# Optimization experiments

Measured on AMD Instinct MI355X. Metric: run time of the kernel, lower is better.

## Reference

```python
import jax, jax.numpy as jnp
import numpy as np

N = 65536      # points
NS = 16        # nsample
CIN = 128
CMID = 128
COUT = 128
S = 8          # share_planes
EPS = 1e-5


def setup_inputs() -> dict:
    key = jax.random.key(0)
    ks = jax.random.split(key, 12)
    f = lambda k, shape, s=0.05: (jax.random.normal(k, shape, jnp.float32) * s)
    inp = {
        'p': jax.random.normal(ks[0], (N, 3), jnp.float32),
        'x': jax.random.normal(ks[1], (N, CIN), jnp.float32),
        'idx': jax.random.randint(ks[2], (N, NS), 0, N, jnp.int32),
        'wq': f(ks[3], (CMID, CIN)), 'bq': jnp.zeros((CMID,), jnp.float32),
        'wk': f(ks[4], (CMID, CIN)), 'bk': jnp.zeros((CMID,), jnp.float32),
        'wv': f(ks[5], (COUT, CIN)), 'bv': jnp.zeros((COUT,), jnp.float32),
        'p_w1': f(ks[6], (3, 3), 0.3), 'p_b1': jnp.zeros((3,), jnp.float32),
        'p_bng': jnp.ones((3,), jnp.float32), 'p_bnb': jnp.zeros((3,), jnp.float32),
        'p_bnm': jnp.zeros((3,), jnp.float32), 'p_bnv': jnp.ones((3,), jnp.float32),
        'p_w2': f(ks[7], (COUT, 3), 0.3), 'p_b2': jnp.zeros((COUT,), jnp.float32),
        'w_bn1g': jnp.ones((CMID,), jnp.float32), 'w_bn1b': jnp.zeros((CMID,), jnp.float32),
        'w_bn1m': jnp.zeros((CMID,), jnp.float32), 'w_bn1v': jnp.ones((CMID,), jnp.float32),
        'w_w1': f(ks[8], (CMID // S, CMID)), 'w_b1': jnp.zeros((CMID // S,), jnp.float32),
        'w_bn2g': jnp.ones((CMID // S,), jnp.float32), 'w_bn2b': jnp.zeros((CMID // S,), jnp.float32),
        'w_bn2m': jnp.zeros((CMID // S,), jnp.float32), 'w_bn2v': jnp.ones((CMID // S,), jnp.float32),
        'w_w2': f(ks[9], (COUT // S, COUT // S)), 'w_b2': jnp.zeros((COUT // S,), jnp.float32),
    }
    return inp


def _bn(t, g, b, m, v):
    # eval-mode BatchNorm1d: per-channel affine on last axis
    return (t - m) * (g / jnp.sqrt(v + EPS)) + b


def reference(p, x, idx, wq, bq, wk, bk, wv, bv,
              p_w1, p_b1, p_bng, p_bnb, p_bnm, p_bnv, p_w2, p_b2,
              w_bn1g, w_bn1b, w_bn1m, w_bn1v, w_w1, w_b1,
              w_bn2g, w_bn2b, w_bn2m, w_bn2v, w_w2, w_b2):
    idx = idx.astype(jnp.int32)
    x_q = x @ wq.T + bq            # (n, mid)
    x_k = x @ wk.T + bk            # (n, mid)
    x_v = x @ wv.T + bv            # (n, out)
    # boundary_queryandgroup: gather neighbors, relative xyz
    p_r = p[idx] - p[:, None, :]   # (n, ns, 3)
    g_k = x_k[idx]                 # (n, ns, mid)
    g_v = x_v[idx]                 # (n, ns, out)
    # linear_p: Linear(3,3) -> BN(3) -> ReLU -> Linear(3,out)
    p_r = p_r @ p_w1.T + p_b1
    p_r = jax.nn.relu(_bn(p_r, p_bng, p_bnb, p_bnm, p_bnv))
    p_r = p_r @ p_w2.T + p_b2      # (n, ns, out)
    n, ns, _ = g_k.shape
    w = g_k - x_q[:, None, :] + p_r.reshape(n, ns, COUT // CMID, CMID).sum(2)
    # linear_w: BN(mid) -> ReLU -> Linear(mid, mid//s) -> BN -> ReLU -> Linear
    w = jax.nn.relu(_bn(w, w_bn1g, w_bn1b, w_bn1m, w_bn1v))
    w = w @ w_w1.T + w_b1          # (n, ns, mid//s)
    w = jax.nn.relu(_bn(w, w_bn2g, w_bn2b, w_bn2m, w_bn2v))
    w = w @ w_w2.T + w_b2          # (n, ns, out//s)
    w = jax.nn.softmax(w, axis=1)  # over neighbors
    out = ((g_v + p_r).reshape(n, ns, S, COUT // S) * w[:, :, None, :]).sum(1)
    return out.reshape(n, COUT)
```

## Files before the change

### kernel.cpp

```cpp
#include <hip/hip_runtime.h>
#include <hip/hip_bf16.h>

typedef unsigned short u16;
typedef unsigned int   u32;
typedef unsigned long long u64;

#define NPTS 65536
#define NNS  16
#define C    128

static __device__ __forceinline__ float bflo(u32 u){ return __builtin_bit_cast(float, u << 16); }
static __device__ __forceinline__ float ldbf(const u16* p){ return bflo((u32)(*p)); }
static __device__ __forceinline__ u16 f2bf(float f){
  u32 u = __builtin_bit_cast(u32, f);
  return (u16)((u + 0x7fffu + ((u >> 16) & 1u)) >> 16);
}
static __device__ __forceinline__ u32 pk2bf(float lo, float hi){
  __hip_bfloat162 h = __float22bfloat162_rn(make_float2(lo, hi));
  u32 r; __builtin_memcpy(&r, &h, sizeof(r));
  return r;
}

template<bool BF>
static __device__ __forceinline__ float ldT(const void* b, long i){
  if constexpr (BF) return ldbf((const u16*)b + i);
  else return ((const float*)b)[i];
}

struct P29 {
  const void *p, *x; const int* idx;
  const void *wq,*bq,*wk,*bk,*wv,*bv;
  const void *pw1,*pb1,*pbng,*pbnb,*pbnm,*pbnv,*pw2,*pb2;
  const void *bn1g,*bn1b,*bn1m,*bn1v,*ww1,*wb1;
  const void *bn2g,*bn2b,*bn2m,*bn2v,*ww2,*wb2;
};

static __device__ int detect_mode(const void* x){
  int lane = threadIdx.x & 63;
  float vb = ldbf((const u16*)x + lane);
  bool okb = (vb == vb) && fabsf(vb) < 32.f && fabsf(vb) > 1e-8f;
  if (__popcll(__ballot(okb)) >= 56) return 0;
  float vf = ((const float*)x)[lane];
  bool okf = (vf == vf) && fabsf(vf) < 32.f && fabsf(vf) > 1e-8f;
  if (__popcll(__ballot(okf)) >= 56) return 1;
  return 2;
}

template<bool BF>
static __device__ int value_checks(const P29& q){
  int lane = threadIdx.x & 63;
  bool ok = fabsf(ldT<BF>(q.bq, lane)) <= 1e-5f;
  ok = ok && fabsf(ldT<BF>(q.bn1v, lane) - 1.f) <= 0.02f;
  if (lane < 3) ok = ok && fabsf(ldT<BF>(q.pbnv, lane) - 1.f) <= 0.02f;
  if (__popcll(__ballot(ok)) != 64) return 4;
  int v = q.idx[lane];
  bool in = (v >= 0 && v < NPTS);
  if (__popcll(__ballot(in)) != 64) return 3;
  bool oz = ((lane & 1) == 1) ? (v == 0) : true;
  if (__popcll(__ballot(oz)) == 64) return 5;
  return 0;
}

static __device__ void report_out(void* outv, float code_val){
  u16* o = (u16*)outv;
  const int tid = threadIdx.x, wid = tid >> 6, lane = tid & 63;
  const int n = blockIdx.x * 4 + wid;
  ((u32*)o)[(size_t)n * 64 + lane] = 0u;
  if (blockIdx.x == 0 && tid == 0){
    ((float*)outv)[0] = code_val;
    o[2] = f2bf(code_val);
  }
}

__global__ __launch_bounds__(256) void report_kernel(void* outv, float code_val){
  report_out(outv, code_val);
}

typedef __bf16 bf16x8 __attribute__((ext_vector_type(8)));
typedef __bf16 bf16x4 __attribute__((ext_vector_type(4)));
typedef short  s16x4  __attribute__((ext_vector_type(4)));
typedef float  f32x4  __attribute__((ext_vector_type(4)));

static __device__ __forceinline__ f32x4 mfma16_bf16(u32 alo, u32 ahi,
                                                    u32 blo, u32 bhi, f32x4 c){
#if __has_builtin(__builtin_amdgcn_mfma_f32_16x16x16_bf16)
  union { u32 u[2]; bf16x4 v; } A, B;
  A.u[0]=alo; A.u[1]=ahi; B.u[0]=blo; B.u[1]=bhi;
  return __builtin_amdgcn_mfma_f32_16x16x16_bf16(A.v, B.v, c, 0, 0, 0);
#else
  union { u32 u[2]; s16x4 v; } A, B;
  A.u[0]=alo; A.u[1]=ahi; B.u[0]=blo; B.u[1]=bhi;
  return __builtin_amdgcn_mfma_f32_16x16x16bf16_1k(A.v, B.v, c, 0, 0, 0);
#endif
}

template<bool BF>
static __device__ __forceinline__ void stage64(const void* src, size_t row0, u16* lds){
  const int t = threadIdx.x;
  #pragma unroll
  for (int i = 0; i < 4; i++){
    const int ch  = t + i * 256;
    const int row = ch >> 4, cc = ch & 15;
    u16 tmp[8];
    if constexpr (BF){
      *(uint4*)tmp = *(const uint4*)((const u16*)src + ((row0 + row) * (size_t)128 + cc * 8));
    } else {
      const float* s = (const float*)src + ((row0 + row) * (size_t)128 + cc * 8);
      float4 a = ((const float4*)s)[0];
      float4 b = ((const float4*)s)[1];
      *(u32*)&tmp[0] = pk2bf(a.x, a.y);
      *(u32*)&tmp[2] = pk2bf(a.z, a.w);
      *(u32*)&tmp[4] = pk2bf(b.x, b.y);
      *(u32*)&tmp[6] = pk2bf(b.z, b.w);
    }
    const u32 byte = (u32)row * 256u + (u32)((cc * 16) ^ ((row & 7) << 4));
    *(uint4*)((char*)lds + byte) = *(uint4*)tmp;
  }
}

template<bool BF>
static __device__ void qkv_mfma_body(const P29 q, u16* xq, u16* xk, u16* xv){
  __shared__ u16 sA[64 * 128];
  const size_t n0 = (size_t)blockIdx.x * 64;

  stage64<BF>(q.x, n0, sA);
  __syncthreads();

  const int tid = threadIdx.x, wid = tid >> 6, lane = tid & 63;
  const int lm = lane & 15, lk = lane >> 4;
  const int chbase = wid * 32;

  #pragma unroll 1
  for (int a = 0; a < 3; a++){
    const void* W  = (a == 0) ? q.wq : (a == 1) ? q.wk : q.wv;
    const void* Bp = (a == 0) ? q.bq : (a == 1) ? q.bk : q.bv;
    u16*       D   = (a == 0) ? xq  : (a == 1) ? xk  : xv;

    bf16x8 wfr[2][4];
    #pragma unroll
    for (int ci = 0; ci < 2; ci++){
      const int ch = chbase + ci*16 + lm;
      #pragma unroll
      for (int kk = 0; kk < 4; kk++){
        const int k0 = kk*32 + lk*8;
        uint4 raw;
        if constexpr (BF){
          raw = *(const uint4*)((const u16*)W + (size_t)ch * C + k0);
        } else {
          const float* s = (const float*)W + (size_t)ch * C + k0;
          float4 x0 = ((const float4*)s)[0], x1 = ((const float4*)s)[1];
          raw.x = pk2bf(x0.x, x0.y); raw.y = pk2bf(x0.z, x0.w);
          raw.z = pk2bf(x1.x, x1.y); raw.w = pk2bf(x1.z, x1.w);
        }
        wfr[ci][kk] = __builtin_bit_cast(bf16x8, raw);
      }
    }

    f32x4 acc[2][4];
    #pragma unroll
    for (int ci = 0; ci < 2; ci++)
      #pragma unroll
      for (int pi = 0; pi < 4; pi++) acc[ci][pi] = f32x4{0.f,0.f,0.f,0.f};

    #pragma unroll
    for (int kk = 0; kk < 4; kk++){
      const u32 kb = (u32)(kk * 64 + lk * 16);
      #pragma unroll
      for (int pi = 0; pi < 4; pi++){
        const u32 row = (u32)(pi*16 + lm);
        bf16x8 xf = *(const bf16x8*)((const char*)sA + row * 256u + (kb ^ ((row & 7u) << 4)));
        acc[0][pi] = __builtin_amdgcn_mfma_f32_16x16x32_bf16(wfr[0][kk], xf, acc[0][pi], 0, 0, 0);
        acc[1][pi] = __builtin_amdgcn_mfma_f32_16x16x32_bf16(wfr[1][kk], xf, acc[1][pi], 0, 0, 0);
      }
    }

    #pragma unroll
    for (int ci = 0; ci < 2; ci++){
      const int chb = chbase + ci*16 + lk*4;
      float b0 = ldT<BF>(Bp, chb+0), b1 = ldT<BF>(Bp, chb+1);
      float b2 = ldT<BF>(Bp, chb+2), b3 = ldT<BF>(Bp, chb+3);
      #pragma unroll
      for (int pi = 0; pi < 4; pi++){
        const size_t n = n0 + (size_t)(pi*16 + lm);
        uint2 pk;
        pk.x = pk2bf(acc[ci][pi][0] + b0, acc[ci][pi][1] + b1);
        pk.y = pk2bf(acc[ci][pi][2] + b2, acc[ci][pi][3] + b3);
        *(uint2*)(D + n * 128 + chb) = pk;
      }
    }
  }
}

__global__ __launch_bounds__(256)
void qkv_kernel(P29 q, u16* xq, u16* xk, u16* xv){
  int mode = detect_mode(q.x);
  if (mode == 0)      qkv_mfma_body<true >(q, xq, xk, xv);
  else if (mode == 1) qkv_mfma_body<false>(q, xq, xk, xv);
}

template<bool BF>
static __device__ void main_body(const P29 q, const u16* xq, const u16* xk,
                                 const u16* xv, void* outv){
  __shared__ char s_buf[4][4352];

  const int tid  = threadIdx.x;
  const int wid  = tid >> 6, lane = tid & 63;
  const int n    = blockIdx.x * 4 + wid;
  const int c0   = lane * 2, c1 = c0 + 1;

  u16*   s_w  = (u16*)  s_buf[wid];
  float* s_wf = (float*) s_buf[wid];
  float* s_q  = (float*)(s_buf[wid] + 4096);

  const float ps0 = ldT<BF>(q.p, (size_t)n*3 + 0);
  const float ps1 = ldT<BF>(q.p, (size_t)n*3 + 1);
  const float ps2 = ldT<BF>(q.p, (size_t)n*3 + 2);

  {
    const int pm = lane >> 2, pt = lane & 3;
    const int ptc = (pt < 3) ? pt : 2;
    int pim = q.idx[n*NNS + pm];
    pim = (pim < 0) ? 0 : ((pim >= NPTS) ? NPTS-1 : pim);
    float ssp = ldT<BF>(q.pbng, ptc) * rsqrtf(fabsf(ldT<BF>(q.pbnv, ptc)) + 1e-5f);
    float ttp = ldT<BF>(q.pbnb, ptc) - ldT<BF>(q.pbnm, ptc) * ssp;
    float w0p = ssp * ldT<BF>(q.pw1, ptc*3 + 0);
    float w1p = ssp * ldT<BF>(q.pw1, ptc*3 + 1);
    float w2p = ssp * ldT<BF>(q.pw1, ptc*3 + 2);
    float pbp = ssp * ldT<BF>(q.pb1, ptc) + ttp;
    float pd0 = ldT<BF>(q.p, (size_t)pim*3 + 0) - ps0;
    float pd1 = ldT<BF>(q.p, (size_t)pim*3 + 1) - ps1;
    float pd2 = ldT<BF>(q.p, (size_t)pim*3 + 2) - ps2;
    s_q[pm*4 + pt] = fmaxf(pd0*w0p + pd1*w1p + pd2*w2p + pbp, 0.f);
  }
  asm volatile("" ::: "memory");

  const float s0 = ldT<BF>(q.bn1g, c0) * rsqrtf(fabsf(ldT<BF>(q.bn1v, c0)) + 1e-5f);
  const float t0 = ldT<BF>(q.bn1b, c0) - ldT<BF>(q.bn1m, c0) * s0;
  const float s1 = ldT<BF>(q.bn1g, c1) * rsqrtf(fabsf(ldT<BF>(q.bn1v, c1)) + 1e-5f);
  const float t1 = ldT<BF>(q.bn1b, c1) - ldT<BF>(q.bn1m, c1) * s1;
  const float A0 = ldT<BF>(q.pw2, c0*3+0), A1 = ldT<BF>(q.pw2, c0*3+1), A2 = ldT<BF>(q.pw2, c0*3+2);
  const float B0 = ldT<BF>(q.pw2, c1*3+0), B1 = ldT<BF>(q.pw2, c1*3+1), B2 = ldT<BF>(q.pw2, c1*3+2);
  const float pbc0 = ldT<BF>(q.pb2, c0), pbc1 = ldT<BF>(q.pb2, c1);
  const u32 xqp = *(const u32*)(xq + (size_t)n * C + c0);
  const float xq0 = bflo(xqp & 0xffffu);
  const float xq1 = bflo(xqp >> 16);

  u32 svp[NNS];
  #pragma unroll
  for (int m = 0; m < NNS; m++){
    int im = q.idx[n*NNS + m];
    im = (im < 0) ? 0 : ((im >= NPTS) ? NPTS-1 : im);
    float q0 = s_q[m*4 + 0];
    float q1 = s_q[m*4 + 1];
    float q2 = s_q[m*4 + 2];
    float pr0 = q0*A0 + q1*A1 + q2*A2 + pbc0;
    float pr1 = q0*B0 + q1*B1 + q2*B2 + pbc1;
    u32 gk = *(const u32*)(xk + (size_t)im * C + c0);
    u32 gv = *(const u32*)(xv + (size_t)im * C + c0);
    float gk0 = bflo(gk & 0xffffu);
    float gk1 = bflo(gk >> 16);
    float w0 = fmaxf(s0*(gk0 - xq0 + pr0) + t0, 0.f);
    float w1 = fmaxf(s1*(gk1 - xq1 + pr1) + t1, 0.f);
    u32 byte = (u32)m * 256u + (((u32)lane * 4u) ^ (((u32)m & 7u) << 4));
    *(u32*)((char*)s_w + byte) = pk2bf(w0, w1);
    float sv0 = bflo(gv & 0xffffu) + pr0;
    float sv1 = bflo(gv >> 16)     + pr1;
    svp[m] = pk2bf(sv0, sv1);
  }
  asm volatile("" ::: "memory");

  const int tb = (lane >> 4) * 4;
  const int lm_ = lane & 15, ug_ = lane >> 4;
  {
    f32x4 acc2;
    #pragma unroll
    for (int r = 0; r < 4; r++) acc2[r] = ldT<BF>(q.wb1, tb + r);
    #pragma unroll
    for (int kk = 0; kk < 4; kk++){
      const int cbase = kk*32 + ug_*8;
      uint4 raw;
      if constexpr (BF){
        raw = *(const uint4*)((const u16*)q.ww1 + (size_t)lm_*C + cbase);
      } else {
        const float* s = (const float*)q.ww1 + (size_t)lm_*C + cbase;
        float4 a = ((const float4*)s)[0], b = ((const float4*)s)[1];
        raw.x = pk2bf(a.x, a.y); raw.y = pk2bf(a.z, a.w);
        raw.z = pk2bf(b.x, b.y); raw.w = pk2bf(b.z, b.w);
      }
      bf16x8 wwA = __builtin_bit_cast(bf16x8, raw);
      const u32 off = ((u32)(kk*64 + ug_*16)) ^ (((u32)lm_ & 7u) << 4);
      bf16x8 bw = *(const bf16x8*)((const char*)s_w + (u32)lm_*256u + off);
      acc2 = __builtin_amdgcn_mfma_f32_16x16x32_bf16(wwA, bw, acc2, 0, 0, 0);
    }
    u32 blo, bhi;
    {
      float mid[4];
      #pragma unroll
      for (int r = 0; r < 4; r++){
        const int t = tb + r;
        float ss = ldT<BF>(q.bn2g, t) * rsqrtf(fabsf(ldT<BF>(q.bn2v, t)) + 1e-5f);
        float tt = ldT<BF>(q.bn2b, t) - ldT<BF>(q.bn2m, t) * ss;
        mid[r] = fmaxf(ss*acc2[r] + tt, 0.f);
      }
      blo = pk2bf(mid[0], mid[1]);
      bhi = pk2bf(mid[2], mid[3]);
    }
    u32 alo, ahi;
    if constexpr (BF){
      uint2 a8 = *(const uint2*)((const u16*)q.ww2 + (size_t)lm_*16 + tb);
      alo = a8.x; ahi = a8.y;
    } else {
      const float* s = (const float*)q.ww2 + (size_t)lm_*16 + tb;
      float4 a = *(const float4*)s;
      alo = pk2bf(a.x, a.y);
      ahi = pk2bf(a.z, a.w);
    }
    f32x4 acc3;
    #pragma unroll
    for (int r = 0; r < 4; r++) acc3[r] = ldT<BF>(q.wb2, tb + r);
    acc3 = mfma16_bf16(alo, ahi, blo, bhi, acc3);
    #pragma unroll
    for (int r = 0; r < 4; r++){
      float v = acc3[r];
      float mx = v;
      #pragma unroll
      for (int msk = 1; msk < 16; msk <<= 1) mx = fmaxf(mx, __shfl_xor(mx, msk, 64));
      float ee = __expf(v - mx);
      float sm = ee;
      #pragma unroll
      for (int msk = 1; msk < 16; msk <<= 1) sm += __shfl_xor(sm, msk, 64);
      s_wf[lm_*17 + tb + r] = ee / sm;
    }
  }
  asm volatile("" ::: "memory");

  float acc0 = 0.f, acc1 = 0.f;
  const int u0 = c0 & 15;
  #pragma unroll
  for (int m = 0; m < NNS; m++){
    float wf0 = s_wf[m*17 + u0];
    float wf1 = s_wf[m*17 + u0 + 1];
    acc0 += bflo(svp[m] & 0xffffu) * wf0;
    acc1 += bflo(svp[m] >> 16)     * wf1;
  }
  if (!(acc0 == acc0)) acc0 = 12345.f;
  if (!(acc1 == acc1)) acc1 = 12345.f;
  if (BF){
    ((u32*)outv)[(size_t)n * 64 + lane] = pk2bf(acc0, acc1);
  } else {
    float* o = (float*)outv;
    o[(size_t)n * C + c0] = acc0;
    o[(size_t)n * C + c1] = acc1;
  }
}

__global__ __launch_bounds__(256)
void main_kernel(P29 q, const u16* xq, const u16* xk, const u16* xv, void* outv){
  int mode = detect_mode(q.x);
  int code = (mode == 2) ? 2 : (mode == 0 ? value_checks<true>(q) : value_checks<false>(q));
  if (code){ report_out(outv, code * 10000.f); return; }
  if (mode == 0) main_body<true >(q, xq, xk, xv, outv);
  else           main_body<false>(q, xq, xk, xv, outv);
}

extern "C" void kernel_launch(void* const* d_in, const int* in_sizes, int n_in,
                              void* d_out, int out_size, void* d_ws, size_t ws_size,
                              hipStream_t stream)
{
  static const int exp_sizes[29] = {
    196608, 8388608, 1048576,
    16384, 128, 16384, 128, 16384, 128,
    9, 3, 3, 3, 3, 3,
    384, 128,
    128, 128, 128, 128,
    2048, 16,
    16, 16, 16, 16,
    256, 16
  };
  int code = 0;
  if (n_in != 29) code = 7;
  else {
    for (int i = 0; i < 29; i++) if (in_sizes[i] != exp_sizes[i]) { code = 8; break; }
  }
  if (!code && out_size != NPTS * C) code = 9;
  if (!code && ws_size < (size_t)3 * NPTS * C * sizeof(u16)) code = 6;

  if (code){
    hipLaunchKernelGGL(report_kernel, dim3(NPTS/4), dim3(256), 0, stream,
                       d_out, (float)(code * 10000));
    return;
  }

  P29 q;
  q.p   = d_in[0];  q.x    = d_in[1];  q.idx  = (const int*)d_in[2];
  q.wq  = d_in[3];  q.bq   = d_in[4];  q.wk   = d_in[5];  q.bk  = d_in[6];
  q.wv  = d_in[7];  q.bv   = d_in[8];
  q.pw1 = d_in[9];  q.pb1  = d_in[10];
  q.pbng= d_in[11]; q.pbnb = d_in[12]; q.pbnm = d_in[13]; q.pbnv= d_in[14];
  q.pw2 = d_in[15]; q.pb2  = d_in[16];
  q.bn1g= d_in[17]; q.bn1b = d_in[18]; q.bn1m = d_in[19]; q.bn1v= d_in[20];
  q.ww1 = d_in[21]; q.wb1  = d_in[22];
  q.bn2g= d_in[23]; q.bn2b = d_in[24]; q.bn2m = d_in[25]; q.bn2v= d_in[26];
  q.ww2 = d_in[27]; q.wb2  = d_in[28];

  u16* xq = (u16*)d_ws;
  u16* xk = xq + (size_t)NPTS * C;
  u16* xv = xk + (size_t)NPTS * C;

  hipLaunchKernelGGL(qkv_kernel, dim3(1024), dim3(256), 0, stream, q, xq, xk, xv);
  hipLaunchKernelGGL(main_kernel, dim3(NPTS/4), dim3(256), 0, stream, q, xq, xk, xv, d_out);
}
```

Measured before the change: 347.8 us.

## Interleave K and V projections into one buffer for single gather loads

The QKV kernel now writes K and V into one interleaved buffer, with groups of four K channels followed by the matching four V channels per row. The main kernel gathers each neighbor row with one 16-byte load per lane instead of two separate 4-byte loads from distant K and V arrays. Each lane then picks its own pair out of the loaded data. This cuts the number of scattered gather transactions and makes each neighbor's K and V share one contiguous segment, at the cost of adjacent lanes loading the same 16 bytes twice.

```diff
diff --git a/kernel.cpp b/kernel.cpp
--- a/kernel.cpp
+++ b/kernel.cpp
@@ -119,7 +119,7 @@
 }
 
 template<bool BF>
-static __device__ void qkv_mfma_body(const P29 q, u16* xq, u16* xk, u16* xv){
+static __device__ void qkv_mfma_body(const P29 q, u16* xq, u16* xkv){
   __shared__ u16 sA[64 * 128];
   const size_t n0 = (size_t)blockIdx.x * 64;
 
@@ -134,7 +134,6 @@
   for (int a = 0; a < 3; a++){
     const void* W  = (a == 0) ? q.wq : (a == 1) ? q.wk : q.wv;
     const void* Bp = (a == 0) ? q.bq : (a == 1) ? q.bk : q.bv;
-    u16*       D   = (a == 0) ? xq  : (a == 1) ? xk  : xv;
 
     bf16x8 wfr[2][4];
     #pragma unroll
@@ -185,22 +184,25 @@
         uint2 pk;
         pk.x = pk2bf(acc[ci][pi][0] + b0, acc[ci][pi][1] + b1);
         pk.y = pk2bf(acc[ci][pi][2] + b2, acc[ci][pi][3] + b3);
-        *(uint2*)(D + n * 128 + chb) = pk;
+        if (a == 0)
+          *(uint2*)(xq + n * 128 + chb) = pk;
+        else
+          *(uint2*)(xkv + n * 256 + (size_t)((chb >> 2) * 8 + (a == 2 ? 4 : 0))) = pk;
       }
     }
   }
 }
 
 __global__ __launch_bounds__(256)
-void qkv_kernel(P29 q, u16* xq, u16* xk, u16* xv){
+void qkv_kernel(P29 q, u16* xq, u16* xkv){
   int mode = detect_mode(q.x);
-  if (mode == 0)      qkv_mfma_body<true >(q, xq, xk, xv);
-  else if (mode == 1) qkv_mfma_body<false>(q, xq, xk, xv);
+  if (mode == 0)      qkv_mfma_body<true >(q, xq, xkv);
+  else if (mode == 1) qkv_mfma_body<false>(q, xq, xkv);
 }
 
 template<bool BF>
-static __device__ void main_body(const P29 q, const u16* xq, const u16* xk,
-                                 const u16* xv, void* outv){
+static __device__ void main_body(const P29 q, const u16* xq, const u16* xkv,
+                                 void* outv){
   __shared__ char s_buf[4][4352];
 
   const int tid  = threadIdx.x;
@@ -244,6 +246,7 @@
   const u32 xqp = *(const u32*)(xq + (size_t)n * C + c0);
   const float xq0 = bflo(xqp & 0xffffu);
   const float xq1 = bflo(xqp >> 16);
+  const bool hi_pair = (lane & 1);
 
   u32 svp[NNS];
   #pragma unroll
@@ -255,8 +258,9 @@
     float q2 = s_q[m*4 + 2];
     float pr0 = q0*A0 + q1*A1 + q2*A2 + pbc0;
     float pr1 = q0*B0 + q1*B1 + q2*B2 + pbc1;
-    u32 gk = *(const u32*)(xk + (size_t)im * C + c0);
-    u32 gv = *(const u32*)(xv + (size_t)im * C + c0);
+    uint4 raw = *(const uint4*)(xkv + (size_t)im * 256 + (size_t)((lane >> 1) * 8));
+    u32 gk = hi_pair ? raw.y : raw.x;
+    u32 gv = hi_pair ? raw.w : raw.z;
     float gk0 = bflo(gk & 0xffffu);
     float gk1 = bflo(gk >> 16);
     float w0 = fmaxf(s0*(gk0 - xq0 + pr0) + t0, 0.f);
@@ -355,12 +359,12 @@
 }
 
 __global__ __launch_bounds__(256)
-void main_kernel(P29 q, const u16* xq, const u16* xk, const u16* xv, void* outv){
+void main_kernel(P29 q, const u16* xq, const u16* xkv, void* outv){
   int mode = detect_mode(q.x);
   int code = (mode == 2) ? 2 : (mode == 0 ? value_checks<true>(q) : value_checks<false>(q));
   if (code){ report_out(outv, code * 10000.f); return; }
-  if (mode == 0) main_body<true >(q, xq, xk, xv, outv);
-  else           main_body<false>(q, xq, xk, xv, outv);
+  if (mode == 0) main_body<true >(q, xq, xkv, outv);
+  else           main_body<false>(q, xq, xkv, outv);
 }
 
 extern "C" void kernel_launch(void* const* d_in, const int* in_sizes, int n_in,
@@ -403,10 +407,9 @@
   q.bn2g= d_in[23]; q.bn2b = d_in[24]; q.bn2m = d_in[25]; q.bn2v= d_in[26];
   q.ww2 = d_in[27]; q.wb2  = d_in[28];
 
-  u16* xq = (u16*)d_ws;
-  u16* xk = xq + (size_t)NPTS * C;
-  u16* xv = xk + (size_t)NPTS * C;
-
-  hipLaunchKernelGGL(qkv_kernel, dim3(1024), dim3(256), 0, stream, q, xq, xk, xv);
-  hipLaunchKernelGGL(main_kernel, dim3(NPTS/4), dim3(256), 0, stream, q, xq, xk, xv, d_out);
-}
+  u16* xq  = (u16*)d_ws;
+  u16* xkv = xq + (size_t)NPTS * C;
+
+  hipLaunchKernelGGL(qkv_kernel, dim3(1024), dim3(256), 0, stream, q, xq, xkv);
+  hipLaunchKernelGGL(main_kernel, dim3(NPTS/4), dim3(256), 0, stream, q, xq, xkv, d_out);
+}
```

Measured after the change: 351.8 us. Within noise of the previous version (+1.2%).
